# Kernel tuning notes

Measured on AMD Instinct MI355X. Metric: run time of the kernel, lower is better.

## Reference

```python
import jax, jax.numpy as jnp
import numpy as np

B, T, H, W, C = 8, 16, 128, 128, 3
PATCH = 8
MODEL_DIM = 512
FFN_DIM = 2048
NUM_BLOCKS = 4
NUM_HEADS = 8
LATENT_DIM = 64
NUM_LATENTS = 4096
ACTION_DIM = 16
PATCH_TOKEN_DIM = C * PATCH * PATCH  # 192


def setup_inputs() -> dict:
    key = jax.random.key(0)
    ks = jax.random.split(key, 12)
    g = lambda k, s: jax.random.normal(k, s, dtype=jnp.float32) * 0.02
    D, L = MODEL_DIM, NUM_BLOCKS
    return dict(
        videos=jax.random.uniform(ks[0], (B, T, H, W, C), dtype=jnp.float32),
        patch_w=g(ks[1], (PATCH_TOKEN_DIM, D)),
        patch_b=jnp.zeros((D,), jnp.float32),
        action_token=g(ks[2], (PATCH_TOKEN_DIM,)),
        ln1_g=jnp.ones((L, D), jnp.float32), ln1_b=jnp.zeros((L, D), jnp.float32),
        wqkv_s=g(ks[3], (L, D, 3 * D)), wo_s=g(ks[4], (L, D, D)),
        ln2_g=jnp.ones((L, D), jnp.float32), ln2_b=jnp.zeros((L, D), jnp.float32),
        wqkv_t=g(ks[5], (L, D, 3 * D)), wo_t=g(ks[6], (L, D, D)),
        ln3_g=jnp.ones((L, D), jnp.float32), ln3_b=jnp.zeros((L, D), jnp.float32),
        mlp_w1=g(ks[7], (L, D, FFN_DIM)), mlp_b1=jnp.zeros((L, FFN_DIM), jnp.float32),
        mlp_w2=g(ks[8], (L, FFN_DIM, D)), mlp_b2=jnp.zeros((L, D), jnp.float32),
        lnf_g=jnp.ones((D,), jnp.float32), lnf_b=jnp.zeros((D,), jnp.float32),
        out_w=g(ks[9], (D, LATENT_DIM)),
        codebook=g(ks[10], (NUM_LATENTS, LATENT_DIM)),
        action_w=g(ks[11], (LATENT_DIM, ACTION_DIM)),
    )


def _ln(x, g, b):
    m = jnp.mean(x, -1, keepdims=True)
    v = jnp.var(x, -1, keepdims=True)
    return (x - m) * jax.lax.rsqrt(v + 1e-5) * g + b


def _mha(x, wqkv, wo, causal):
    bsz, S, D = x.shape
    hd = D // NUM_HEADS
    q, k, v = jnp.split(x @ wqkv, 3, axis=-1)
    split = lambda t: t.reshape(bsz, S, NUM_HEADS, hd).transpose(0, 2, 1, 3)
    q, k, v = split(q), split(k), split(v)
    scores = jnp.einsum('bhqd,bhkd->bhqk', q, k) * (1.0 / np.sqrt(hd))
    if causal:
        mask = jnp.tril(jnp.ones((S, S), dtype=bool))
        scores = jnp.where(mask, scores, jnp.finfo(scores.dtype).min)
    o = jnp.einsum('bhqk,bhkd->bhqd', jax.nn.softmax(scores, axis=-1), v)
    return o.transpose(0, 2, 1, 3).reshape(bsz, S, D) @ wo


def _forward(videos, patch_w, patch_b, action_token, ln1_g, ln1_b, wqkv_s, wo_s,
             ln2_g, ln2_b, wqkv_t, wo_t, ln3_g, ln3_b, mlp_w1, mlp_b1, mlp_w2,
             mlp_b2, lnf_g, lnf_b, out_w, codebook, action_w):
    b, t = videos.shape[:2]
    hp, wp = H // PATCH, W // PATCH
    # patchify: (B,T,H,W,C) -> (B,T,N,p*p*C)
    x = videos.reshape(b, t, hp, PATCH, wp, PATCH, C)
    x = x.transpose(0, 1, 2, 4, 3, 5, 6).reshape(b, t, hp * wp, PATCH_TOKEN_DIM)
    # prepend learned action token per frame
    act = jnp.broadcast_to(action_token, (b, t, 1, PATCH_TOKEN_DIM))
    x = jnp.concatenate([act, x], axis=2)             # (B,T,S,Ep)
    S = x.shape[2]
    tok = x @ patch_w + patch_b                        # (B,T,S,D)
    for i in range(NUM_BLOCKS):
        # spatial attention within each frame
        h = _ln(tok, ln1_g[i], ln1_b[i]).reshape(b * t, S, MODEL_DIM)
        tok = tok + _mha(h, wqkv_s[i], wo_s[i], causal=False).reshape(b, t, S, MODEL_DIM)
        # temporal causal attention per spatial position
        h = _ln(tok, ln2_g[i], ln2_b[i]).transpose(0, 2, 1, 3).reshape(b * S, t, MODEL_DIM)
        h = _mha(h, wqkv_t[i], wo_t[i], causal=True)
        tok = tok + h.reshape(b, S, t, MODEL_DIM).transpose(0, 2, 1, 3)
        # MLP
        h = _ln(tok, ln3_g[i], ln3_b[i])
        tok = tok + jax.nn.gelu(h @ mlp_w1[i] + mlp_b1[i]) @ mlp_w2[i] + mlp_b2[i]
    tok = _ln(tok, lnf_g, lnf_b)
    # latent action per transition: action token of frames 1..T-1
    z = tok[:, 1:, 0, :] @ out_w                       # (B, T-1, latent_dim)
    # VQ: nearest-neighbor codebook lookup (squared-L2 argmin + gather)
    d = (jnp.sum(z * z, -1, keepdims=True)
         - 2.0 * (z @ codebook.T)
         + jnp.sum(codebook * codebook, -1))           # (B, T-1, num_latents)
    idx = jnp.argmin(d, axis=-1)                       # (B, T-1)
    z_q = codebook[idx]
    z_q = z + jax.lax.stop_gradient(z_q - z)           # straight-through
    latent_actions = jax.lax.stop_gradient(z_q)
    return latent_actions @ action_w                   # (B, T-1, action_dim)


def reference(videos, patch_w, patch_b, action_token, ln1_g, ln1_b, wqkv_s, wo_s,
              ln2_g, ln2_b, wqkv_t, wo_t, ln3_g, ln3_b, mlp_w1, mlp_b1, mlp_w2,
              mlp_b2, lnf_g, lnf_b, out_w, codebook, action_w):
    return _forward(videos, patch_w, patch_b, action_token, ln1_g, ln1_b, wqkv_s,
                    wo_s, ln2_g, ln2_b, wqkv_t, wo_t, ln3_g, ln3_b, mlp_w1,
                    mlp_b1, mlp_w2, mlp_b2, lnf_g, lnf_b, out_w, codebook, action_w)
```

## Files before the change

kernel.cpp:

```cpp
#include <hip/hip_runtime.h>
#include <hip/hip_bf16.h>

#define B_ 8
#define T_ 16
#define S_ 257
#define D_ 512
#define FFN_ 2048
#define NH_ 8
#define HD_ 64
#define PTD_ 192
#define NTOK (B_*T_*S_)
#define CH 4112
#define PCH 8224
#define WSCALE 64.0f
#define WINV 0.015625f

typedef unsigned int uint;
typedef unsigned short ushort;
typedef __attribute__((ext_vector_type(8))) _Float16 half8;
typedef __attribute__((ext_vector_type(4))) float f32x4;

__device__ __forceinline__ float warp_rsum(float v){
#pragma unroll
  for (int m = 32; m >= 1; m >>= 1) v += __shfl_xor(v, m);
  return v;
}
__device__ __forceinline__ float gelu_f(float x){
  float x3 = x*x*x;
  return 0.5f*x*(1.0f + tanhf(0.7978845608028654f*(x + 0.044715f*x3)));
}
__device__ __forceinline__ void split_f16(float f, ushort& h, ushort& l){
  _Float16 hh = (_Float16)f;
  float hf = (float)hh;
  _Float16 ll = (_Float16)(f - hf);
  h = __builtin_bit_cast(ushort, hh);
  l = __builtin_bit_cast(ushort, ll);
}
__device__ __forceinline__ ushort to_f16u(float f){
  return __builtin_bit_cast(ushort, (_Float16)f);
}
__device__ __forceinline__ float from_f16u(ushort u){
  return (float)__builtin_bit_cast(_Float16, u);
}
__device__ __forceinline__ void gload16(const ushort* g, ushort* l){
  __builtin_amdgcn_global_load_lds(
      (const __attribute__((address_space(1))) void*)(g),
      (__attribute__((address_space(3))) void*)(l),
      16, 0, 0);
}

__global__ __launch_bounds__(256) void ln_single(
    const float* __restrict__ x, const float* __restrict__ g,
    const float* __restrict__ bb, ushort* __restrict__ aH)
{
  int row = blockIdx.x * 4 + (threadIdx.x >> 6);
  int lane = threadIdx.x & 63;
  const float* xr = x + (long)row * D_;
  float4 u0 = *(const float4*)(xr + lane * 8);
  float4 u1 = *(const float4*)(xr + lane * 8 + 4);
  float s = u0.x + u0.y + u0.z + u0.w + u1.x + u1.y + u1.z + u1.w;
  s = warp_rsum(s);
  float mean = s * (1.0f / 512.0f);
  float d[8] = {u0.x - mean, u0.y - mean, u0.z - mean, u0.w - mean,
                u1.x - mean, u1.y - mean, u1.z - mean, u1.w - mean};
  float ss = 0.f;
#pragma unroll
  for (int i = 0; i < 8; i++) ss = fmaf(d[i], d[i], ss);
  ss = warp_rsum(ss);
  float rstd = rsqrtf(ss * (1.0f / 512.0f) + 1e-5f);
  int c = lane * 8;
  float4 g0 = *(const float4*)(g + c), g1 = *(const float4*)(g + c + 4);
  float4 b0 = *(const float4*)(bb + c), b1 = *(const float4*)(bb + c + 4);
  float y[8] = {d[0]*rstd*g0.x + b0.x, d[1]*rstd*g0.y + b0.y,
                d[2]*rstd*g0.z + b0.z, d[3]*rstd*g0.w + b0.w,
                d[4]*rstd*g1.x + b1.x, d[5]*rstd*g1.y + b1.y,
                d[6]*rstd*g1.z + b1.z, d[7]*rstd*g1.w + b1.w};
  ushort h[8];
#pragma unroll
  for (int i = 0; i < 8; i++) h[i] = to_f16u(y[i]);
  uint4 hv = make_uint4((uint)h[0] | ((uint)h[1] << 16), (uint)h[2] | ((uint)h[3] << 16),
                        (uint)h[4] | ((uint)h[5] << 16), (uint)h[6] | ((uint)h[7] << 16));
  *(uint4*)(aH + (long)row * 512 + c) = hv;
}

__global__ __launch_bounds__(256) void convert_w(
    const float* __restrict__ W, ushort* __restrict__ Whi, ushort* __restrict__ Wlo,
    int N, int K)
{
  __shared__ float Tt[64][65];
  const int tid = threadIdx.x;
  const int k0 = blockIdx.x << 6, n0 = blockIdx.y << 6;
  {
    int kk = tid >> 2, nb = (tid & 3) << 4;
#pragma unroll
    for (int q = 0; q < 4; q++) {
      float4 v = *(const float4*)(W + (long)(k0 + kk) * N + n0 + nb + 4 * q);
      Tt[kk][nb + 4*q + 0] = v.x; Tt[kk][nb + 4*q + 1] = v.y;
      Tt[kk][nb + 4*q + 2] = v.z; Tt[kk][nb + 4*q + 3] = v.w;
    }
  }
  __syncthreads();
  {
    int nn = tid >> 2, kb = (tid & 3) << 4;
    uint hw[8], lw[8];
#pragma unroll
    for (int q = 0; q < 8; q++) {
      float a = Tt[kb + 2*q][nn] * WSCALE, b = Tt[kb + 2*q + 1][nn] * WSCALE;
      ushort ha, la, hb, lb;
      split_f16(a, ha, la); split_f16(b, hb, lb);
      hw[q] = (uint)ha | ((uint)hb << 16); lw[q] = (uint)la | ((uint)lb << 16);
    }
    ushort* dh = Whi + (long)(n0 + nn) * K + k0 + kb;
    ushort* dl = Wlo + (long)(n0 + nn) * K + k0 + kb;
    ((uint4*)dh)[0] = make_uint4(hw[0], hw[1], hw[2], hw[3]);
    ((uint4*)dh)[1] = make_uint4(hw[4], hw[5], hw[6], hw[7]);
    ((uint4*)dl)[0] = make_uint4(lw[0], lw[1], lw[2], lw[3]);
    ((uint4*)dl)[1] = make_uint4(lw[4], lw[5], lw[6], lw[7]);
  }
}

template<int BM, int BN, int TM, int TN, int AMODE, bool ASPLIT, bool BSPLIT, bool BIAS, bool GELU, bool RESID, int SOUT>
__global__ __launch_bounds__(256) void gemm_mfma(
    const ushort* __restrict__ aHp, const ushort* __restrict__ aLp, int lda,
    const ushort* __restrict__ wtH, const ushort* __restrict__ wtL, int ldb,
    const float* __restrict__ bias, float* __restrict__ C,
    ushort* __restrict__ coH, ushort* __restrict__ vOut,
    const float* __restrict__ videos, const float* __restrict__ atok,
    int M, int N, int K)
{
  constexpr int NWC = BN / (TN * 16);
  constexpr int NBUF = (AMODE == 0) ? 2 : 1;
  __shared__ __align__(16) ushort sAh[NBUF * BM * 32];
  __shared__ __align__(16) ushort sAl[(AMODE == 1) ? 128 * 32 : 8];
  __shared__ __align__(16) ushort sBh[NBUF * BN * 32];
  __shared__ __align__(16) ushort sBl[BSPLIT ? NBUF * BN * 32 : 8];
  const int tid = threadIdx.x;
  int m0, n0;
  if (AMODE == 0) {
    const int gx = gridDim.x, gy = gridDim.y;
    const int nwg = gx * gy;
    const int o = blockIdx.y * gx + blockIdx.x;
    const int q = nwg >> 3, r = nwg & 7;
    const int xcd = o & 7, idx = o >> 3;
    const int wgid = (xcd < r ? xcd * (q + 1) : r * (q + 1) + (xcd - r) * q) + idx;
    const int mi = wgid / gy, ni = wgid - mi * gy;
    m0 = mi * BM; n0 = ni * BN;
  } else {
    m0 = blockIdx.x * BM; n0 = blockIdx.y * BN;
  }
  const int wid = tid >> 6, lane = tid & 63;
  const int lrow = lane & 15, lkg = lane >> 4;
  const int wr = wid / NWC, wc = wid % NWC;
  const int wrb = wr * TM * 16, wcb = wc * TN * 16;
  f32x4 acc[TM][TN];
#pragma unroll
  for (int mi = 0; mi < TM; mi++)
#pragma unroll
    for (int ni = 0; ni < TN; ni++) acc[mi][ni] = (f32x4){0.f, 0.f, 0.f, 0.f};

  if (AMODE == 0) {
    auto stage = [&](int k0, int d) {
      {
        int row = tid >> 2, cp = tid & 3;
        int csrc = cp ^ ((row >> 1) & 3);
        int ar = m0 + row; if (ar > M - 1) ar = M - 1;
        gload16(aHp + (long)ar * lda + k0 + csrc * 8, &sAh[d * (BM * 32) + tid * 8]);
      }
      if constexpr (BM == 128) {
        int chunk = tid + 256;
        int row = chunk >> 2, cp = chunk & 3;
        int csrc = cp ^ ((row >> 1) & 3);
        int ar = m0 + row; if (ar > M - 1) ar = M - 1;
        gload16(aHp + (long)ar * lda + k0 + csrc * 8, &sAh[d * (BM * 32) + chunk * 8]);
      }
      if (BN == 128) {
#pragma unroll
        for (int i = 0; i < 2; i++) {
          int chunk = tid + 256 * i;
          int row = chunk >> 2, cp = chunk & 3;
          int csrc = cp ^ ((row >> 1) & 3);
          gload16(wtH + (long)(n0 + row) * ldb + k0 + csrc * 8, &sBh[d * 4096 + chunk * 8]);
        }
      } else {
        int chunk = tid;
        int row = chunk >> 2, cp = chunk & 3;
        int csrc = cp ^ ((row >> 1) & 3);
        gload16(wtH + (long)(n0 + row) * ldb + k0 + csrc * 8, &sBh[d * 2048 + chunk * 8]);
        if (BSPLIT)
          gload16(wtL + (long)(n0 + row) * ldb + k0 + csrc * 8, &sBl[d * 2048 + chunk * 8]);
      }
    };
    const int nt = K >> 5;
    stage(0, 0);
    if (nt > 1) stage(32, 1);
    constexpr int LPS = ((BM == 128) ? 2 : 1) + ((BN == 128) ? 2 : (BSPLIT ? 2 : 1));
    for (int t = 0; t < nt; t++) {
      const int cur = t & 1;
      if (t + 1 < nt) {
        if constexpr (LPS == 4) {
          asm volatile("s_waitcnt vmcnt(4)" ::: "memory");
        } else if constexpr (LPS == 3) {
          asm volatile("s_waitcnt vmcnt(3)" ::: "memory");
        } else {
          asm volatile("s_waitcnt vmcnt(2)" ::: "memory");
        }
      } else {
        asm volatile("s_waitcnt vmcnt(0)" ::: "memory");
      }
      __builtin_amdgcn_s_barrier();
      const int aBase = cur * (BM * 32);
      const int bBase = cur * ((BN == 128) ? 4096 : 2048);
      half8 aHf[TM], bHf[TN], bLf[BSPLIT ? TN : 1];
#pragma unroll
      for (int mi = 0; mi < TM; mi++) {
        int ar = wrb + mi * 16 + lrow;
        int ac = (ar * 4 + (lkg ^ ((ar >> 1) & 3))) * 8;
        aHf[mi] = *(const half8*)&sAh[aBase + ac];
      }
#pragma unroll
      for (int ni = 0; ni < TN; ni++) {
        int br = wcb + ni * 16 + lrow;
        int bc = (br * 4 + (lkg ^ ((br >> 1) & 3))) * 8;
        bHf[ni] = *(const half8*)&sBh[bBase + bc];
        if (BSPLIT) bLf[ni] = *(const half8*)&sBl[bBase + bc];
      }
      asm volatile("s_waitcnt lgkmcnt(0)" ::: "memory");
      __builtin_amdgcn_sched_barrier(0);
      __builtin_amdgcn_s_barrier();
      if (t + 2 < nt) stage((t + 2) << 5, cur);
      __builtin_amdgcn_s_setprio(1);
#pragma unroll
      for (int ni = 0; ni < TN; ni++) {
        if (BSPLIT) {
#pragma unroll
          for (int mi = 0; mi < TM; mi++)
            acc[mi][ni] = __builtin_amdgcn_mfma_f32_16x16x32_f16(aHf[mi], bLf[ni], acc[mi][ni], 0, 0, 0);
        }
#pragma unroll
        for (int mi = 0; mi < TM; mi++)
          acc[mi][ni] = __builtin_amdgcn_mfma_f32_16x16x32_f16(aHf[mi], bHf[ni], acc[mi][ni], 0, 0, 0);
      }
      __builtin_amdgcn_s_setprio(0);
      __builtin_amdgcn_sched_barrier(0);
    }
  } else {
    const int rowa = tid >> 1, kba = (tid & 1) << 4;
    const int cb0 = (tid & 1) * 2;
    const int swa = (rowa >> 1) & 3;
    int bt_p = 0, s_p = 0;
    { int ar = m0 + rowa; bt_p = ar / 257; s_p = ar - bt_p * 257; }
    for (int k0 = 0; k0 < K; k0 += 32) {
      float4 vr[4];
#pragma unroll
      for (int q = 0; q < 4; q++) vr[q] = make_float4(0.f, 0.f, 0.f, 0.f);
#pragma unroll
      for (int q = 0; q < 4; q++) {
        int e4 = k0 + kba + 4 * q;
        if (s_p == 0) {
          vr[q] = *(const float4*)(atok + e4);
        } else {
          int p = s_p - 1, ph = p >> 4, pw = p & 15;
          int iq = e4 / 24, jc = e4 - iq * 24;
          vr[q] = *(const float4*)(videos + (long)bt_p * 49152 +
                                   (long)(ph * 8 + iq) * 384 + pw * 24 + jc);
        }
      }
      uint hw[8], lw[8];
#pragma unroll
      for (int q = 0; q < 4; q++) {
        ushort h0,l0,h1,l1,h2,l2,h3,l3;
        split_f16(vr[q].x, h0, l0); split_f16(vr[q].y, h1, l1);
        split_f16(vr[q].z, h2, l2); split_f16(vr[q].w, h3, l3);
        hw[2*q]   = (uint)h0 | ((uint)h1 << 16); lw[2*q]   = (uint)l0 | ((uint)l1 << 16);
        hw[2*q+1] = (uint)h2 | ((uint)h3 << 16); lw[2*q+1] = (uint)l2 | ((uint)l3 << 16);
      }
      *(uint4*)&sAh[(rowa * 4 + (cb0 ^ swa)) * 8]       = make_uint4(hw[0], hw[1], hw[2], hw[3]);
      *(uint4*)&sAh[(rowa * 4 + ((cb0 + 1) ^ swa)) * 8] = make_uint4(hw[4], hw[5], hw[6], hw[7]);
      *(uint4*)&sAl[(rowa * 4 + (cb0 ^ swa)) * 8]       = make_uint4(lw[0], lw[1], lw[2], lw[3]);
      *(uint4*)&sAl[(rowa * 4 + ((cb0 + 1) ^ swa)) * 8] = make_uint4(lw[4], lw[5], lw[6], lw[7]);
      {
#pragma unroll
        for (int i = 0; i < 2; i++) {
          int chunk = tid + 256 * i;
          int row = chunk >> 2, cp = chunk & 3;
          int csrc = cp ^ ((row >> 1) & 3);
          gload16(wtH + (long)(n0 + row) * ldb + k0 + csrc * 8, &sBh[chunk * 8]);
          if (BSPLIT)
            gload16(wtL + (long)(n0 + row) * ldb + k0 + csrc * 8, &sBl[chunk * 8]);
        }
      }
      __syncthreads();
      half8 aHf[TM], aLf[TM];
#pragma unroll
      for (int mi = 0; mi < TM; mi++) {
        int ar = wrb + mi * 16 + lrow;
        int ac = (ar * 4 + (lkg ^ ((ar >> 1) & 3))) * 8;
        aHf[mi] = *(const half8*)&sAh[ac];
        if (ASPLIT) aLf[mi] = *(const half8*)&sAl[ac];
      }
#pragma unroll
      for (int ni = 0; ni < TN; ni++) {
        int br = wcb + ni * 16 + lrow;
        int bc = (br * 4 + (lkg ^ ((br >> 1) & 3))) * 8;
        half8 bH = *(const half8*)&sBh[bc];
#pragma unroll
        for (int mi = 0; mi < TM; mi++) {
          if (ASPLIT)
            acc[mi][ni] = __builtin_amdgcn_mfma_f32_16x16x32_f16(aLf[mi], bH, acc[mi][ni], 0, 0, 0);
        }
        if (BSPLIT) {
          half8 bL = *(const half8*)&sBl[bc];
#pragma unroll
          for (int mi = 0; mi < TM; mi++)
            acc[mi][ni] = __builtin_amdgcn_mfma_f32_16x16x32_f16(aHf[mi], bL, acc[mi][ni], 0, 0, 0);
        }
#pragma unroll
        for (int mi = 0; mi < TM; mi++)
          acc[mi][ni] = __builtin_amdgcn_mfma_f32_16x16x32_f16(aHf[mi], bH, acc[mi][ni], 0, 0, 0);
      }
      __syncthreads();
    }
  }
#pragma unroll
  for (int mi = 0; mi < TM; mi++) {
    int rowg = m0 + wrb + mi * 16 + lkg * 4;
#pragma unroll
    for (int j = 0; j < 4; j++) {
      int r = rowg + j;
      if (r < M) {
#pragma unroll
        for (int ni = 0; ni < TN; ni++) {
          int cg = n0 + wcb + ni * 16 + lrow;
          float v = acc[mi][ni][j] * WINV;
          if (BIAS) v += bias[cg];
          if (GELU) v = gelu_f(v);
          if (SOUT == 2) {
            coH[(long)r * N + cg] = to_f16u(v);
          } else if (SOUT == 3) {
            if (cg < 1024) coH[(long)r * 1024 + cg] = to_f16u(v);
            else           vOut[(long)r * 512 + (cg - 1024)] = to_f16u(v);
          } else {
            long idx = (long)r * N + cg;
            if (RESID) C[idx] += v; else C[idx] = v;
          }
        }
      }
    }
  }
}

__global__ __launch_bounds__(256) void flash_spatial(
    const ushort* __restrict__ qk, const ushort* __restrict__ v2,
    ushort* __restrict__ ctxc)
{
  __shared__ __align__(16) ushort sQ[64*72];
  __shared__ __align__(16) ushort sK[64*72];
  __shared__ __align__(16) ushort sV[64*72];
  __shared__ __align__(16) ushort sP[64*72];
  const int tid = threadIdx.x;
  const int wid = tid >> 6, lane = tid & 63;
  const int lr = lane & 15, lg = lane >> 4;
  const int fh = blockIdx.y;
  const int fl = fh >> 3, hh = fh & 7;
  const int q0 = blockIdx.x * 64;
  const long rbase = (long)fl * S_;
  const int srow = tid >> 2, sc0 = (tid & 3) << 4;

  {
    int gr = q0 + srow;
    uint4 h0 = make_uint4(0,0,0,0), h1 = h0;
    if (gr < S_) {
      const ushort* sh = qk + (rbase + gr) * 1024 + hh * HD_ + sc0;
      h0 = ((const uint4*)sh)[0]; h1 = ((const uint4*)sh)[1];
    }
    uint4* dh = (uint4*)&sQ[srow*72 + sc0];
    dh[0] = h0; dh[1] = h1;
  }
  __syncthreads();
  half8 qH[2];
  {
    int qrl = wid * 16 + lr;
#pragma unroll
    for (int s = 0; s < 2; s++)
      qH[s] = *(const half8*)&sQ[qrl*72 + s*32 + lg*8];
  }
  f32x4 accS[5][4];
#pragma unroll
  for (int t = 0; t < 5; t++)
#pragma unroll
    for (int kc = 0; kc < 4; kc++) accS[t][kc] = (f32x4){0.f,0.f,0.f,0.f};

#pragma unroll
  for (int t = 0; t < 5; t++) {
    __syncthreads();
    {
      int gr = t*64 + srow;
      uint4 h0 = make_uint4(0,0,0,0), h1 = h0;
      if (gr < S_) {
        const ushort* sh = qk + (rbase + gr) * 1024 + 512 + hh * HD_ + sc0;
        h0 = ((const uint4*)sh)[0]; h1 = ((const uint4*)sh)[1];
      }
      uint4* dh = (uint4*)&sK[srow*72 + sc0];
      dh[0] = h0; dh[1] = h1;
    }
    __syncthreads();
#pragma unroll
    for (int s = 0; s < 2; s++) {
#pragma unroll
      for (int kc = 0; kc < 4; kc++) {
        int off = (kc*16 + lr)*72 + s*32 + lg*8;
        half8 bH = *(const half8*)&sK[off];
        accS[t][kc] = __builtin_amdgcn_mfma_f32_16x16x32_f16(qH[s], bH, accS[t][kc], 0,0,0);
      }
    }
  }

  float m[4] = {-3.0e38f, -3.0e38f, -3.0e38f, -3.0e38f};
#pragma unroll
  for (int t = 0; t < 5; t++)
#pragma unroll
    for (int kc = 0; kc < 4; kc++) {
      int kcol = t*64 + kc*16 + lr;
      if (kcol < S_) {
#pragma unroll
        for (int j = 0; j < 4; j++) m[j] = fmaxf(m[j], accS[t][kc][j] * 0.125f);
      }
    }
#pragma unroll
  for (int mk = 8; mk >= 1; mk >>= 1)
#pragma unroll
    for (int j = 0; j < 4; j++) m[j] = fmaxf(m[j], __shfl_xor(m[j], mk));
  float l[4] = {0.f, 0.f, 0.f, 0.f};
#pragma unroll
  for (int t = 0; t < 5; t++)
#pragma unroll
    for (int kc = 0; kc < 4; kc++) {
      int kcol = t*64 + kc*16 + lr;
#pragma unroll
      for (int j = 0; j < 4; j++) {
        float p = (kcol < S_) ? expf(accS[t][kc][j]*0.125f - m[j]) : 0.f;
        accS[t][kc][j] = p;
        l[j] += p;
      }
    }
#pragma unroll
  for (int mk = 8; mk >= 1; mk >>= 1)
#pragma unroll
    for (int j = 0; j < 4; j++) l[j] += __shfl_xor(l[j], mk);

  f32x4 accO[4];
#pragma unroll
  for (int dc = 0; dc < 4; dc++) accO[dc] = (f32x4){0.f,0.f,0.f,0.f};
#pragma unroll
  for (int t = 0; t < 5; t++) {
#pragma unroll
    for (int kc = 0; kc < 4; kc++)
#pragma unroll
      for (int j = 0; j < 4; j++) {
        int addr = (wid*16 + lg*4 + j)*72 + kc*16 + lr;
        sP[addr] = to_f16u(accS[t][kc][j]);
      }
    __syncthreads();
    {
      int gr = t*64 + srow;
      ushort tmp[16];
      uint4 a = make_uint4(0,0,0,0), b = a;
      if (gr < S_) {
        const ushort* src = v2 + (rbase + gr) * 512 + hh * HD_ + sc0;
        a = ((const uint4*)src)[0]; b = ((const uint4*)src)[1];
      }
      *(uint4*)&tmp[0] = a; *(uint4*)&tmp[8] = b;
#pragma unroll
      for (int e = 0; e < 16; e++) sV[(sc0 + e)*72 + srow] = tmp[e];
    }
    __syncthreads();
#pragma unroll
    for (int s = 0; s < 2; s++) {
      int poff = (wid*16 + lr)*72 + s*32 + lg*8;
      half8 pH = *(const half8*)&sP[poff];
#pragma unroll
      for (int dc = 0; dc < 4; dc++) {
        int voff = (dc*16 + lr)*72 + s*32 + lg*8;
        half8 vH = *(const half8*)&sV[voff];
        accO[dc] = __builtin_amdgcn_mfma_f32_16x16x32_f16(pH, vH, accO[dc], 0,0,0);
      }
    }
  }
#pragma unroll
  for (int j = 0; j < 4; j++) {
    int grow = q0 + wid*16 + lg*4 + j;
    if (grow < S_) {
      float inv = 1.0f / l[j];
#pragma unroll
      for (int dc = 0; dc < 4; dc++) {
        float o = accO[dc][j] * inv;
        long idx = (rbase + grow) * 512 + hh*64 + dc*16 + lr;
        ctxc[idx] = to_f16u(o);
      }
    }
  }
}

__global__ __launch_bounds__(64) void temporal_attn(
    const ushort* __restrict__ qk, const ushort* __restrict__ v2,
    ushort* __restrict__ ctxc)
{
  const int gid = blockIdx.x;
  const int b2 = gid / (S_ * NH_);
  const int rem = gid - b2 * S_ * NH_;
  const int hh = rem & 7;
  const int s = rem >> 3;
  const int lane = threadIdx.x;
  __shared__ float Qs[16][65];
  __shared__ float Ks[16][65];
  __shared__ float Pm[16][17];
  float v[16];
  const long rbase = (long)b2 * CH + s;
#pragma unroll
  for (int t = 0; t < 16; t++) {
    long row = rbase + (long)t * S_;
    long qoff = row * 1024 + hh * HD_ + lane;
    Qs[t][lane] = from_f16u(qk[qoff]);
    Ks[t][lane] = from_f16u(qk[qoff + 512]);
    v[t] = from_f16u(v2[row * 512 + hh * HD_ + lane]);
  }
  __syncthreads();
  const int rq = lane >> 2, c0 = lane & 3;
  float sc[4];
#pragma unroll
  for (int j = 0; j < 4; j++) {
    int c = c0 + (j << 2);
    if (c <= rq) {
      float d = 0.f;
#pragma unroll
      for (int k = 0; k < 64; k++) d = fmaf(Qs[rq][k], Ks[c][k], d);
      sc[j] = d * 0.125f;
    } else sc[j] = -3.0e38f;
  }
  float mx = fmaxf(fmaxf(sc[0], sc[1]), fmaxf(sc[2], sc[3]));
  mx = fmaxf(mx, __shfl_xor(mx, 1));
  mx = fmaxf(mx, __shfl_xor(mx, 2));
  float sum = 0.f;
#pragma unroll
  for (int j = 0; j < 4; j++) { sc[j] = expf(sc[j] - mx); sum += sc[j]; }
  sum += __shfl_xor(sum, 1);
  sum += __shfl_xor(sum, 2);
  float inv = 1.0f / sum;
#pragma unroll
  for (int j = 0; j < 4; j++) Pm[rq][c0 + (j << 2)] = sc[j] * inv;
  __syncthreads();
#pragma unroll
  for (int t = 0; t < 16; t++) {
    float o = 0.f;
#pragma unroll
    for (int k = 0; k < 16; k++) o = fmaf(Pm[t][k], v[k], o);
    long idx = (rbase + (long)t * S_) * 512 + hh * HD_ + lane;
    ctxc[idx] = to_f16u(o);
  }
}

__global__ __launch_bounds__(1024) void final_vq(
    const float* __restrict__ tok, const float* __restrict__ lnf_g,
    const float* __restrict__ lnf_b, const float* __restrict__ out_w,
    const float* __restrict__ codebook, const float* __restrict__ action_w,
    float* __restrict__ out)
{
  __shared__ float xs[512];
  __shared__ float red[16];
  __shared__ float zp[1024];
  __shared__ float zs[64];
  __shared__ float bd[16];
  __shared__ int   bi[16];
  __shared__ int   bsel;
  const int b = blockIdx.x / 15, tm = blockIdx.x % 15;
  const int tid = threadIdx.x;
  const int wv = tid >> 6, lane = tid & 63;
  const float* xr = tok + ((long)(b * T_ + tm + 1) * S_) * D_;
  float x0 = (tid < 512) ? xr[tid] : 0.f;
  float s = warp_rsum(x0);
  if (lane == 0) red[wv] = s;
  __syncthreads();
  float tot = 0.f;
#pragma unroll
  for (int w = 0; w < 16; w++) tot += red[w];
  float mean = tot * (1.0f / 512.0f);
  float dv = (tid < 512) ? (x0 - mean) : 0.f;
  __syncthreads();
  float ss = warp_rsum(dv * dv);
  if (lane == 0) red[wv] = ss;
  __syncthreads();
  float vtot = 0.f;
#pragma unroll
  for (int w = 0; w < 16; w++) vtot += red[w];
  float rstd = rsqrtf(vtot * (1.0f / 512.0f) + 1e-5f);
  if (tid < 512) xs[tid] = dv * rstd * lnf_g[tid] + lnf_b[tid];
  __syncthreads();
  {
    int o = tid & 63, p = tid >> 6;
    int d0 = p * 32;
    float z = 0.f;
#pragma unroll 8
    for (int k = 0; k < 32; k++) z = fmaf(xs[d0 + k], out_w[(long)(d0 + k) * 64 + o], z);
    zp[tid] = z;
  }
  __syncthreads();
  if (tid < 64) {
    float z = 0.f;
#pragma unroll
    for (int p = 0; p < 16; p++) z += zp[p * 64 + tid];
    zs[tid] = z;
  }
  __syncthreads();
  float best = 3.0e38f; int bidx = 0;
  for (int c = tid; c < 4096; c += 1024) {
    const float4* cp = (const float4*)(codebook + (long)c * 64);
    float dot = 0.f, cn = 0.f;
#pragma unroll
    for (int k = 0; k < 16; k++) {
      float4 w = cp[k];
      dot = fmaf(zs[4*k + 0], w.x, dot); cn = fmaf(w.x, w.x, cn);
      dot = fmaf(zs[4*k + 1], w.y, dot); cn = fmaf(w.y, w.y, cn);
      dot = fmaf(zs[4*k + 2], w.z, dot); cn = fmaf(w.z, w.z, cn);
      dot = fmaf(zs[4*k + 3], w.w, dot); cn = fmaf(w.w, w.w, cn);
    }
    float dist = cn - 2.0f * dot;
    if (dist < best) { best = dist; bidx = c; }
  }
#pragma unroll
  for (int mk = 32; mk >= 1; mk >>= 1) {
    float ob = __shfl_xor(best, mk);
    int   oi = __shfl_xor(bidx, mk);
    if (ob < best || (ob == best && oi < bidx)) { best = ob; bidx = oi; }
  }
  if (lane == 0) { bd[wv] = best; bi[wv] = bidx; }
  __syncthreads();
  if (tid == 0) {
    float bb = bd[0]; int ii = bi[0];
#pragma unroll
    for (int w = 1; w < 16; w++)
      if (bd[w] < bb || (bd[w] == bb && bi[w] < ii)) { bb = bd[w]; ii = bi[w]; }
    bsel = ii;
  }
  __syncthreads();
  int idx = bsel;
  if (tid < 16) {
    const float* cp = codebook + (long)idx * 64;
    float o = 0.f;
#pragma unroll
    for (int k = 0; k < 64; k++) o = fmaf(cp[k], action_w[k * 16 + tid], o);
    out[((long)(b * 15 + tm)) * 16 + tid] = o;
  }
}

extern "C" void kernel_launch(void* const* d_in, const int* in_sizes, int n_in,
                              void* d_out, int out_size, void* d_ws, size_t ws_size,
                              hipStream_t stream)
{
  const float* videos       = (const float*)d_in[0];
  const float* patch_w      = (const float*)d_in[1];
  const float* patch_b      = (const float*)d_in[2];
  const float* action_token = (const float*)d_in[3];
  const float* ln1_g  = (const float*)d_in[4];
  const float* ln1_b  = (const float*)d_in[5];
  const float* wqkv_s = (const float*)d_in[6];
  const float* wo_s   = (const float*)d_in[7];
  const float* ln2_g  = (const float*)d_in[8];
  const float* ln2_b  = (const float*)d_in[9];
  const float* wqkv_t = (const float*)d_in[10];
  const float* wo_t   = (const float*)d_in[11];
  const float* ln3_g  = (const float*)d_in[12];
  const float* ln3_b  = (const float*)d_in[13];
  const float* mlp_w1 = (const float*)d_in[14];
  const float* mlp_b1 = (const float*)d_in[15];
  const float* mlp_w2 = (const float*)d_in[16];
  const float* mlp_b2 = (const float*)d_in[17];
  const float* lnf_g  = (const float*)d_in[18];
  const float* lnf_b  = (const float*)d_in[19];
  const float* out_w  = (const float*)d_in[20];
  const float* codebook = (const float*)d_in[21];
  const float* action_w = (const float*)d_in[22];
  float* out = (float*)d_out;

  float* ws    = (float*)d_ws;
  float* tok   = ws;
  ushort* wt1h = (ushort*)(ws + 16842752);
  ushort* wt1l = wt1h + 1048576;
  ushort* wt2h = (ushort*)(ws + 17891328);
  ushort* wt2l = wt2h + 1048576;
  ushort* aH   = (ushort*)(ws + 18939904);
  ushort* qk   = (ushort*)(ws + 21045248);
  ushort* v2   = (ushort*)(ws + 25255936);
  ushort* ctx  = (ushort*)(ws + 27361280);
  ushort* mid  = qk;

  convert_w<<<dim3(3, 8), 256, 0, stream>>>(patch_w, wt1h, wt1l, 512, 192);
  gemm_mfma<128,128,4,4,1,true,true,true,false,false,0><<<dim3(257, 4), 256, 0, stream>>>(
      nullptr, nullptr, 0, wt1h, wt1l, 192, patch_b, tok, nullptr, nullptr,
      videos, action_token, NTOK, 512, 192);

  for (int L = 0; L < 4; L++) {
    convert_w<<<dim3(8, 24), 256, 0, stream>>>(wqkv_s + (long)L*512*1536, wt1h, wt1l, 1536, 512);
    convert_w<<<dim3(8, 8),  256, 0, stream>>>(wo_s   + (long)L*512*512,  wt2h, wt2l, 512, 512);
    for (int pr = 0; pr < 4; pr++) {
      long r0 = (long)pr * PCH;
      ln_single<<<PCH / 4, 256, 0, stream>>>(tok + r0 * D_, ln1_g + L*512, ln1_b + L*512, aH);
      gemm_mfma<64,128,2,4,0,false,false,false,false,false,3><<<dim3(129, 12), 256, 0, stream>>>(
          aH, nullptr, 512, wt1h, wt1l, 512, nullptr, nullptr,
          qk, v2, nullptr, nullptr, PCH, 1536, 512);
      flash_spatial<<<dim3(5, 256), 256, 0, stream>>>(qk, v2, ctx);
      gemm_mfma<64,64,1,4,0,false,false,false,false,true,0><<<dim3(129, 8), 256, 0, stream>>>(
          ctx, nullptr, 512, wt2h, wt2l, 512, nullptr, tok + r0 * D_,
          nullptr, nullptr, nullptr, nullptr, PCH, 512, 512);
    }
    convert_w<<<dim3(8, 24), 256, 0, stream>>>(wqkv_t + (long)L*512*1536, wt1h, wt1l, 1536, 512);
    convert_w<<<dim3(8, 8),  256, 0, stream>>>(wo_t   + (long)L*512*512,  wt2h, wt2l, 512, 512);
    for (int pr = 0; pr < 4; pr++) {
      long r0 = (long)pr * PCH;
      ln_single<<<PCH / 4, 256, 0, stream>>>(tok + r0 * D_, ln2_g + L*512, ln2_b + L*512, aH);
      gemm_mfma<64,128,2,4,0,false,false,false,false,false,3><<<dim3(129, 12), 256, 0, stream>>>(
          aH, nullptr, 512, wt1h, wt1l, 512, nullptr, nullptr,
          qk, v2, nullptr, nullptr, PCH, 1536, 512);
      temporal_attn<<<2 * S_ * NH_, 64, 0, stream>>>(qk, v2, ctx);
      gemm_mfma<64,64,1,4,0,false,false,false,false,true,0><<<dim3(129, 8), 256, 0, stream>>>(
          ctx, nullptr, 512, wt2h, wt2l, 512, nullptr, tok + r0 * D_,
          nullptr, nullptr, nullptr, nullptr, PCH, 512, 512);
    }
    convert_w<<<dim3(8, 32), 256, 0, stream>>>(mlp_w1 + (long)L*512*2048, wt1h, wt1l, 2048, 512);
    convert_w<<<dim3(32, 8), 256, 0, stream>>>(mlp_w2 + (long)L*2048*512, wt2h, wt2l, 512, 2048);
    for (int c = 0; c < 4; c++) {
      long m0r = (long)c * PCH;
      ln_single<<<PCH / 4, 256, 0, stream>>>(tok + m0r * D_, ln3_g + L*512, ln3_b + L*512, aH);
      gemm_mfma<64,128,2,4,0,false,false,true,true,false,2><<<dim3(129, 16), 256, 0, stream>>>(
          aH, nullptr, 512, wt1h, wt1l, 512, mlp_b1 + (long)L*2048, nullptr, mid, nullptr,
          nullptr, nullptr, PCH, FFN_, 512);
      gemm_mfma<64,64,1,4,0,false,false,true,false,true,0><<<dim3(129, 8), 256, 0, stream>>>(
          mid, nullptr, 2048, wt2h, wt2l, 2048, mlp_b2 + (long)L*512, tok + m0r * D_,
          nullptr, nullptr, nullptr, nullptr, PCH, 512, 2048);
    }
  }

  final_vq<<<B_ * (T_ - 1), 1024, 0, stream>>>(tok, lnf_g, lnf_b, out_w, codebook, action_w, out);
}
```

Before: 3.832 ms.

## Prefetch K/V tiles into registers and remap spatial attention grid

In the spatial flash-attention kernel, the next K and V tiles are now loaded from global memory into registers (double-buffered) while the current tile is being processed. This hides global load latency behind the MFMA and softmax work. The 2D grid becomes a 1D grid with a swizzled block-to-(frame, head, q-tile) mapping, which interleaves heads across neighbouring blocks and likely changes L2 locality and XCD distribution. It adds register pressure, which could lower occupancy.

```diff
diff --git a/kernel.cpp b/kernel.cpp
--- a/kernel.cpp
+++ b/kernel.cpp
@@ -360,9 +360,10 @@
   const int tid = threadIdx.x;
   const int wid = tid >> 6, lane = tid & 63;
   const int lr = lane & 15, lg = lane >> 4;
-  const int fh = blockIdx.y;
+  const int o = blockIdx.x;
+  const int fh = ((o & 7) << 5) | ((o >> 3) & 31);
   const int fl = fh >> 3, hh = fh & 7;
-  const int q0 = blockIdx.x * 64;
+  const int q0 = (o >> 8) * 64;
   const long rbase = (long)fl * S_;
   const int srow = tid >> 2, sc0 = (tid & 3) << 4;
 
@@ -376,6 +377,14 @@
     uint4* dh = (uint4*)&sQ[srow*72 + sc0];
     dh[0] = h0; dh[1] = h1;
   }
+  uint4 kh0[2], kh1[2];
+  {
+    kh0[0] = make_uint4(0,0,0,0); kh1[0] = kh0[0];
+    if (srow < S_) {
+      const ushort* sh = qk + (rbase + srow) * 1024 + 512 + hh * HD_ + sc0;
+      kh0[0] = ((const uint4*)sh)[0]; kh1[0] = ((const uint4*)sh)[1];
+    }
+  }
   __syncthreads();
   half8 qH[2];
   {
@@ -392,16 +401,19 @@
 
 #pragma unroll
   for (int t = 0; t < 5; t++) {
+    if (t < 4) {
+      int nb = (t + 1) & 1;
+      int gr = (t + 1) * 64 + srow;
+      kh0[nb] = make_uint4(0,0,0,0); kh1[nb] = kh0[nb];
+      if (gr < S_) {
+        const ushort* sh = qk + (rbase + gr) * 1024 + 512 + hh * HD_ + sc0;
+        kh0[nb] = ((const uint4*)sh)[0]; kh1[nb] = ((const uint4*)sh)[1];
+      }
+    }
     __syncthreads();
     {
-      int gr = t*64 + srow;
-      uint4 h0 = make_uint4(0,0,0,0), h1 = h0;
-      if (gr < S_) {
-        const ushort* sh = qk + (rbase + gr) * 1024 + 512 + hh * HD_ + sc0;
-        h0 = ((const uint4*)sh)[0]; h1 = ((const uint4*)sh)[1];
-      }
       uint4* dh = (uint4*)&sK[srow*72 + sc0];
-      dh[0] = h0; dh[1] = h1;
+      dh[0] = kh0[t & 1]; dh[1] = kh1[t & 1];
     }
     __syncthreads();
 #pragma unroll
@@ -415,6 +427,15 @@
     }
   }
 
+  uint4 vh0[2], vh1[2];
+  {
+    vh0[0] = make_uint4(0,0,0,0); vh1[0] = vh0[0];
+    if (srow < S_) {
+      const ushort* src = v2 + (rbase + srow) * 512 + hh * HD_ + sc0;
+      vh0[0] = ((const uint4*)src)[0]; vh1[0] = ((const uint4*)src)[1];
+    }
+  }
+
   float m[4] = {-3.0e38f, -3.0e38f, -3.0e38f, -3.0e38f};
 #pragma unroll
   for (int t = 0; t < 5; t++)
@@ -453,6 +474,15 @@
   for (int dc = 0; dc < 4; dc++) accO[dc] = (f32x4){0.f,0.f,0.f,0.f};
 #pragma unroll
   for (int t = 0; t < 5; t++) {
+    if (t < 4) {
+      int nb = (t + 1) & 1;
+      int gr = (t + 1) * 64 + srow;
+      vh0[nb] = make_uint4(0,0,0,0); vh1[nb] = vh0[nb];
+      if (gr < S_) {
+        const ushort* src = v2 + (rbase + gr) * 512 + hh * HD_ + sc0;
+        vh0[nb] = ((const uint4*)src)[0]; vh1[nb] = ((const uint4*)src)[1];
+      }
+    }
 #pragma unroll
     for (int kc = 0; kc < 4; kc++)
 #pragma unroll
@@ -462,14 +492,8 @@
       }
     __syncthreads();
     {
-      int gr = t*64 + srow;
       ushort tmp[16];
-      uint4 a = make_uint4(0,0,0,0), b = a;
-      if (gr < S_) {
-        const ushort* src = v2 + (rbase + gr) * 512 + hh * HD_ + sc0;
-        a = ((const uint4*)src)[0]; b = ((const uint4*)src)[1];
-      }
-      *(uint4*)&tmp[0] = a; *(uint4*)&tmp[8] = b;
+      *(uint4*)&tmp[0] = vh0[t & 1]; *(uint4*)&tmp[8] = vh1[t & 1];
 #pragma unroll
       for (int e = 0; e < 16; e++) sV[(sc0 + e)*72 + srow] = tmp[e];
     }
@@ -493,9 +517,9 @@
       float inv = 1.0f / l[j];
 #pragma unroll
       for (int dc = 0; dc < 4; dc++) {
-        float o = accO[dc][j] * inv;
+        float o2 = accO[dc][j] * inv;
         long idx = (rbase + grow) * 512 + hh*64 + dc*16 + lr;
-        ctxc[idx] = to_f16u(o);
+        ctxc[idx] = to_f16u(o2);
       }
     }
   }
@@ -707,7 +731,7 @@
       gemm_mfma<64,128,2,4,0,false,false,false,false,false,3><<<dim3(129, 12), 256, 0, stream>>>(
           aH, nullptr, 512, wt1h, wt1l, 512, nullptr, nullptr,
           qk, v2, nullptr, nullptr, PCH, 1536, 512);
-      flash_spatial<<<dim3(5, 256), 256, 0, stream>>>(qk, v2, ctx);
+      flash_spatial<<<dim3(1280), 256, 0, stream>>>(qk, v2, ctx);
       gemm_mfma<64,64,1,4,0,false,false,false,false,true,0><<<dim3(129, 8), 256, 0, stream>>>(
           ctx, nullptr, 512, wt2h, wt2l, 512, nullptr, tok + r0 * D_,
           nullptr, nullptr, nullptr, nullptr, PCH, 512, 512);
```

New measurement: 3.704 ms. 3.4% less time.
